# Kernel tuning notes

Measured on AMD Instinct MI355X. Metric: run time of the kernel, lower is better.

## Reference

```python
import jax, jax.numpy as jnp
import numpy as np

INPUT_WINDOW = 2048
HEAD_DIM = 128  # embedding_size // number_of_heads = 2048 // 16
TAU = 1.0
SCALE = 1.0 / ((INPUT_WINDOW * HEAD_DIM) ** 0.5 * TAU)


def setup_inputs() -> dict:
    key = jax.random.key(0)
    # (batch, number_of_series, length_input_window, hidden_dimensionality)
    x = jax.random.normal(key, (8, 16, 2048, 128), dtype=jnp.float32)
    return {"x": x}


def reference(x) -> jnp.ndarray:
    # Q = K = V = x; scores: [B, S, W, W]
    qk = jnp.einsum("bswd,bsud->bswu", x, x) * SCALE
    attn = jax.nn.softmax(qk, axis=-1)
    # dropout(p=0.1) is identity in eval mode
    out = jnp.einsum("bswu,bsud->bswd", attn, x)
    return out
```

## Files before the change

### kernel.cpp

```cpp
#include <hip/hip_runtime.h>
#include <hip/hip_bf16.h>
#include <utility>


#define NSEQ   2048
#define DIM    128
#define KVBLK  32
#define TILES  (NSEQ / KVBLK)
#define IMG    (KVBLK * DIM)
#define EC (1.44269504088896f / 512.0f)

typedef short s8v __attribute__((ext_vector_type(8)));
typedef float f4   __attribute__((ext_vector_type(4)));
typedef float f8v  __attribute__((ext_vector_type(8)));
typedef float f16v __attribute__((ext_vector_type(16)));
typedef unsigned int u2 __attribute__((ext_vector_type(2)));
typedef unsigned int u4 __attribute__((ext_vector_type(4)));

typedef __attribute__((address_space(1))) const void glob_t;
typedef __attribute__((address_space(3))) void lds_t;

__device__ __forceinline__ unsigned pk2(float a, float b) {
    union { __hip_bfloat162 h; unsigned u; } c;
    c.h = __float22bfloat162_rn(make_float2(a, b));
    return c.u;
}
__device__ __forceinline__ int swz32k(int r) { return ((r & 7) ^ ((r >> 3) & 3)) << 3; }
__device__ __forceinline__ int swz(int r) { return ((r & 7) ^ ((r >> 3) & 7)) << 3; }

__global__ __launch_bounds__(256)
void prepass(const float* __restrict__ x, short* __restrict__ wsK,
             short* __restrict__ wsV) {
    const int b = blockIdx.x;
    const float* src = x + (size_t)b * (64 * DIM);
    short* dK = wsK + (size_t)b * 2 * IMG;
    short* dV = wsV + (size_t)b * 2 * IMG;
    const int rw = threadIdx.x >> 4;
    const int cg = threadIdx.x & 15;
    const int tile = rw >> 3;
    const int ul   = 4 * (rw & 7);

    f4 ld[8];
    const float* s = src + (size_t)(4 * rw) * DIM + 8 * cg;
#pragma unroll
    for (int i = 0; i < 4; ++i) {
        ld[2*i]   = *(const f4*)(s + i * DIM);
        ld[2*i+1] = *(const f4*)(s + i * DIM + 4);
    }
#pragma unroll
    for (int i = 0; i < 4; ++i) {
        const int rl = ul + i;
        u4 kv = { pk2(ld[2*i][0],   ld[2*i][1]),   pk2(ld[2*i][2],   ld[2*i][3]),
                  pk2(ld[2*i+1][0], ld[2*i+1][1]), pk2(ld[2*i+1][2], ld[2*i+1][3]) };
        *(u4*)&dK[tile * IMG + ((rl * DIM + 8 * cg) ^ swz32k(rl))] = kv;
    }
#pragma unroll
    for (int j = 0; j < 8; ++j) {
        const int d  = 8 * cg + j;
        const int hi = j >> 2, jj = j & 3;
        u2 vv = { pk2(ld[0 + hi][jj], ld[2 + hi][jj]),
                  pk2(ld[4 + hi][jj], ld[6 + hi][jj]) };
        *(u2*)&dV[tile * IMG + ((d * KVBLK + ul) ^ swz32k(d))] = vv;
    }
}

__global__ __launch_bounds__(256, 3)
void attn_k32p(const float* __restrict__ x, const short* __restrict__ wsK,
               const short* __restrict__ wsV, float* __restrict__ out) {
    const int bid  = blockIdx.x;
    const int wg   = (bid & 7) * 256 + (bid >> 3);
    const int head = wg >> 4;
    const int qb   = wg & 15;

    float* __restrict__ oh = out + (size_t)head * (NSEQ * DIM);
    const short* gK = wsK + (size_t)head * TILES * IMG;
    const short* gV = wsV + (size_t)head * TILES * IMG;

    const int tid  = threadIdx.x;
    const int lane = tid & 63;
    const int wave = tid >> 6;
    const int l31  = lane & 31;
    const int h    = lane >> 5;

    __shared__ __align__(16) short sK [2][IMG];
    __shared__ __align__(16) short sVt[2][IMG];

    const int qw0 = qb * 128 + wave * 32;
    s8v Qf[8];
    {
        const float* qp = x + (size_t)head * (NSEQ * DIM)
                            + (size_t)(qw0 + l31) * DIM + 8 * h;
#pragma unroll
        for (int ks = 0; ks < 8; ++ks) {
            f4 a = *(const f4*)(qp + ks * 16);
            f4 b = *(const f4*)(qp + ks * 16 + 4);
            u4 q = { pk2(a[0] * EC, a[1] * EC), pk2(a[2] * EC, a[3] * EC),
                     pk2(b[0] * EC, b[1] * EC), pk2(b[2] * EC, b[3] * EC) };
            Qf[ks] = *(s8v*)&q;
        }
    }

    f16v accO[4];
#pragma unroll
    for (int dt = 0; dt < 4; ++dt) accO[dt] = (f16v)(0.f);
    float lsum = 0.f;

    const int soff = wave * 1024 + lane * 8;
    auto stage = [&](int b, int t) {
        const short* srcK = gK + (size_t)t * IMG + soff;
        const short* srcV = gV + (size_t)t * IMG + soff;
#pragma unroll
        for (int i = 0; i < 2; ++i) {
            __builtin_amdgcn_global_load_lds((glob_t*)(srcK + i * 512),
                (lds_t*)&sK[b][soff + i * 512], 16, 0, 0);
            __builtin_amdgcn_global_load_lds((glob_t*)(srcV + i * 512),
                (lds_t*)&sVt[b][soff + i * 512], 16, 0, 0);
        }
    };

    stage(0, 0);
    __syncthreads();

    const int kbase = l31 * DIM + 8 * h;
    const int ksz   = swz32k(l31);

    auto body = [&](auto Bc, int T) {
        constexpr int B = decltype(Bc)::value;
        if (T + 1 < TILES) stage(B ^ 1, T + 1);

        f16v aA = (f16v)(0.f), aB = (f16v)(0.f);
        __builtin_amdgcn_s_setprio(1);
#pragma unroll
        for (int ks = 0; ks < 4; ++ks) {
            s8v Kf0 = *(const s8v*)&sK[B][(kbase + (2 * ks)     * 16) ^ ksz];
            s8v Kf1 = *(const s8v*)&sK[B][(kbase + (2 * ks + 1) * 16) ^ ksz];
            aA = __builtin_amdgcn_mfma_f32_32x32x16_bf16(Kf0, Qf[2*ks],   aA, 0, 0, 0);
            aB = __builtin_amdgcn_mfma_f32_32x32x16_bf16(Kf1, Qf[2*ks+1], aB, 0, 0, 0);
        }
        __builtin_amdgcn_s_setprio(0);

        float part0 = 0.f, part1 = 0.f;
        f8v P0, P1;
#pragma unroll
        for (int r = 0; r < 8; ++r) {
            float v = __builtin_amdgcn_exp2f(aA[r] + aB[r]);
            P0[r] = v; part0 += v;
        }
        s8v Pf0;
        {
            unsigned x0 = pk2(P0[0], P0[1]), x1 = pk2(P0[2], P0[3]);
            unsigned y0 = pk2(P0[4], P0[5]), y1 = pk2(P0[6], P0[7]);
            auto t0 = __builtin_amdgcn_permlane32_swap(x0, y0, false, false);
            auto t1 = __builtin_amdgcn_permlane32_swap(x1, y1, false, false);
            u4 w = { (unsigned)t0[0], (unsigned)t1[0], (unsigned)t0[1], (unsigned)t1[1] };
            Pf0 = *(s8v*)&w;
        }

        __builtin_amdgcn_s_setprio(1);
#pragma unroll
        for (int dt = 0; dt < 4; ++dt) {
            const int d = dt * 32 + l31;
            s8v Vf = *(const s8v*)&sVt[B][(d * KVBLK + 8 * h) ^ swz32k(d)];
            accO[dt] = __builtin_amdgcn_mfma_f32_32x32x16_bf16(Pf0, Vf, accO[dt], 0, 0, 0);
        }
        __builtin_amdgcn_s_setprio(0);

#pragma unroll
        for (int r = 0; r < 8; ++r) {
            float v = __builtin_amdgcn_exp2f(aA[8 + r] + aB[8 + r]);
            P1[r] = v; part1 += v;
        }
        s8v Pf1;
        {
            unsigned x0 = pk2(P1[0], P1[1]), x1 = pk2(P1[2], P1[3]);
            unsigned y0 = pk2(P1[4], P1[5]), y1 = pk2(P1[6], P1[7]);
            auto t0 = __builtin_amdgcn_permlane32_swap(x0, y0, false, false);
            auto t1 = __builtin_amdgcn_permlane32_swap(x1, y1, false, false);
            u4 w = { (unsigned)t0[0], (unsigned)t1[0], (unsigned)t0[1], (unsigned)t1[1] };
            Pf1 = *(s8v*)&w;
        }
        lsum += part0 + part1;

        __builtin_amdgcn_s_setprio(1);
#pragma unroll
        for (int dt = 0; dt < 4; ++dt) {
            const int d = dt * 32 + l31;
            s8v Vf = *(const s8v*)&sVt[B][(d * KVBLK + 8 * h + 16) ^ swz32k(d)];
            accO[dt] = __builtin_amdgcn_mfma_f32_32x32x16_bf16(Pf1, Vf, accO[dt], 0, 0, 0);
        }
        __builtin_amdgcn_s_setprio(0);

        __syncthreads();
    };

    for (int tt = 0; tt < TILES; tt += 2) {
        body(std::integral_constant<int, 0>{}, tt);
        body(std::integral_constant<int, 1>{}, tt + 1);
    }

    const float tot = lsum + __shfl_xor(lsum, 32);
    const float inv = 1.f / tot;
#pragma unroll
    for (int r = 0; r < 16; ++r) {
        const int q      = (r & 3) + 8 * (r >> 2) + 4 * h;
        const float invq = __shfl(inv, q, 32);
        float* op = oh + (size_t)(qw0 + q) * DIM + l31;
#pragma unroll
        for (int dt = 0; dt < 4; ++dt)
            op[dt * 32] = accO[dt][r] * invq;
    }
}

__global__ __launch_bounds__(256, 2)
void attn_fwd_fb(const float* __restrict__ x, float* __restrict__ out) {
    const int bid  = blockIdx.x;
    const int wg   = (bid & 7) * 256 + (bid >> 3);
    const int head = wg >> 4;
    const int qb   = wg & 15;
    const float* __restrict__ xh = x   + (size_t)head * (NSEQ * DIM);
    float* __restrict__       oh = out + (size_t)head * (NSEQ * DIM);
    const int tid  = threadIdx.x;
    const int lane = tid & 63;
    const int wave = tid >> 6;
    const int l31  = lane & 31;
    const int h    = lane >> 5;
    __shared__ __align__(16) short sK [64 * DIM];
    __shared__ __align__(16) short sVt[DIM * 64];
    const int qw0 = qb * 128 + wave * 32;
    s8v Qf[8];
    {
        const float* qp = xh + (size_t)(qw0 + l31) * DIM + 8 * h;
#pragma unroll
        for (int ks = 0; ks < 8; ++ks) {
            f4 a = *(const f4*)(qp + ks * 16);
            f4 b = *(const f4*)(qp + ks * 16 + 4);
            u4 q = { pk2(a[0] * EC, a[1] * EC), pk2(a[2] * EC, a[3] * EC),
                     pk2(b[0] * EC, b[1] * EC), pk2(b[2] * EC, b[3] * EC) };
            Qf[ks] = *(s8v*)&q;
        }
    }
    f16v accO[4];
#pragma unroll
    for (int dt = 0; dt < 4; ++dt) accO[dt] = (f16v)(0.f);
    float lsum = 0.f;
    const int rw = tid >> 4;
    const int cg = tid & 15;
    f4 ld[8];
    {
        const float* s = xh + (size_t)(4 * rw) * DIM + 8 * cg;
#pragma unroll
        for (int i = 0; i < 4; ++i) {
            ld[2*i]   = *(const f4*)(s + i * DIM);
            ld[2*i+1] = *(const f4*)(s + i * DIM + 4);
        }
    }
    for (int kv0 = 0; kv0 < NSEQ; kv0 += 64) {
#pragma unroll
        for (int i = 0; i < 4; ++i) {
            const int r = 4 * rw + i;
            u4 kv = { pk2(ld[2*i][0],   ld[2*i][1]),   pk2(ld[2*i][2],   ld[2*i][3]),
                      pk2(ld[2*i+1][0], ld[2*i+1][1]), pk2(ld[2*i+1][2], ld[2*i+1][3]) };
            *(u4*)&sK[(r * DIM + 8 * cg) ^ swz(r)] = kv;
        }
#pragma unroll
        for (int j = 0; j < 8; ++j) {
            const int d  = 8 * cg + j;
            const int hi = j >> 2, jj = j & 3;
            u2 vv = { pk2(ld[0 + hi][jj], ld[2 + hi][jj]),
                      pk2(ld[4 + hi][jj], ld[6 + hi][jj]) };
            *(u2*)&sVt[(d * 64 + 4 * rw) ^ swz(d)] = vv;
        }
        __syncthreads();
        f16v accS[2];
        accS[0] = (f16v)(0.f); accS[1] = (f16v)(0.f);
        __builtin_amdgcn_s_setprio(1);
#pragma unroll
        for (int ut = 0; ut < 2; ++ut) {
            const int r    = ut * 32 + l31;
            const int base = r * DIM + 8 * h;
            const int sz   = swz(r);
#pragma unroll
            for (int ks = 0; ks < 8; ++ks) {
                s8v Kf = *(const s8v*)&sK[(base + ks * 16) ^ sz];
                accS[ut] = __builtin_amdgcn_mfma_f32_32x32x16_bf16(
                    Kf, Qf[ks], accS[ut], 0, 0, 0);
            }
        }
        __builtin_amdgcn_s_setprio(0);
        if (kv0 + 64 < NSEQ) {
            const float* s = xh + (size_t)(kv0 + 64 + 4 * rw) * DIM + 8 * cg;
#pragma unroll
            for (int i = 0; i < 4; ++i) {
                ld[2*i]   = *(const f4*)(s + i * DIM);
                ld[2*i+1] = *(const f4*)(s + i * DIM + 4);
            }
        }
        float part = 0.f;
#pragma unroll
        for (int ut = 0; ut < 2; ++ut)
#pragma unroll
            for (int r = 0; r < 16; ++r) {
                float v = __builtin_amdgcn_exp2f(accS[ut][r]);
                accS[ut][r] = v;
                part += v;
            }
        lsum += part;
        s8v Pf[4];
#pragma unroll
        for (int ks = 0; ks < 4; ++ks) {
#define PP(f) accS[(f) >> 4][(f) & 15]
            unsigned pa0 = pk2(PP(8*ks + 0), PP(8*ks + 1));
            unsigned pa1 = pk2(PP(8*ks + 2), PP(8*ks + 3));
            unsigned pb0 = pk2(PP(8*ks + 4), PP(8*ks + 5));
            unsigned pb1 = pk2(PP(8*ks + 6), PP(8*ks + 7));
#undef PP
            auto t0 = __builtin_amdgcn_permlane32_swap(pa0, pb0, false, false);
            auto t1 = __builtin_amdgcn_permlane32_swap(pa1, pb1, false, false);
            u4 w = { (unsigned)t0[0], (unsigned)t1[0], (unsigned)t0[1], (unsigned)t1[1] };
            Pf[ks] = *(s8v*)&w;
        }
        __builtin_amdgcn_s_setprio(1);
#pragma unroll
        for (int dt = 0; dt < 4; ++dt) {
            const int d    = dt * 32 + l31;
            const int base = d * 64 + 8 * h;
            const int sz   = swz(d);
#pragma unroll
            for (int ks = 0; ks < 4; ++ks) {
                s8v Vf = *(const s8v*)&sVt[(base + ks * 16) ^ sz];
                accO[dt] = __builtin_amdgcn_mfma_f32_32x32x16_bf16(
                    Pf[ks], Vf, accO[dt], 0, 0, 0);
            }
        }
        __builtin_amdgcn_s_setprio(0);
        __syncthreads();
    }
    const float tot = lsum + __shfl_xor(lsum, 32);
    const float inv = 1.f / tot;
#pragma unroll
    for (int r = 0; r < 16; ++r) {
        const int q      = (r & 3) + 8 * (r >> 2) + 4 * h;
        const float invq = __shfl(inv, q, 32);
        float* op = oh + (size_t)(qw0 + q) * DIM + l31;
#pragma unroll
        for (int dt = 0; dt < 4; ++dt)
            op[dt * 32] = accO[dt][r] * invq;
    }
}

extern "C" void kernel_launch(void* const* d_in, const int* in_sizes, int n_in,
                              void* d_out, int out_size, void* d_ws, size_t ws_size,
                              hipStream_t stream) {
    const float* x = (const float*)d_in[0];
    float* out     = (float*)d_out;
    const size_t perImg = (size_t)128 * TILES * IMG;
    const size_t need   = 2 * perImg * sizeof(short);
    if (ws_size >= need) {
        short* wsK = (short*)d_ws;
        short* wsV = wsK + perImg;
        hipLaunchKernelGGL(prepass, dim3(4096), dim3(256), 0, stream, x, wsK, wsV);
        hipLaunchKernelGGL(attn_k32p, dim3(2048), dim3(256), 0, stream, x, wsK, wsV, out);
    } else {
        hipLaunchKernelGGL(attn_fwd_fb, dim3(2048), dim3(256), 0, stream, x, out);
    }
}
```

Baseline: 363.7 us.

## Software-pipeline QK^T of next tile with softmax and PV of current tile

Restructures the attention loop so the QK^T MFMAs for tile T+1 are interleaved with the exp2 and PV MFMAs of tile T, with a prologue and epilogue to match. K and V staging are split so K is prefetched two tiles ahead and V one tile ahead. The goal is to hide exp/VALU latency behind matrix-core work and lengthen the load prefetch distance. In exchange it keeps two score accumulators live, which raises register pressure at an occupancy of 3 waves per SIMD, and it drops the split aA/aB accumulators in favour of one dependent MFMA chain.

Result: faster. 354.3 us (-2.6%).

```diff
diff --git a/kernel.cpp b/kernel.cpp
--- a/kernel.cpp
+++ b/kernel.cpp
@@ -12,7 +12,6 @@
 
 typedef short s8v __attribute__((ext_vector_type(8)));
 typedef float f4   __attribute__((ext_vector_type(4)));
-typedef float f8v  __attribute__((ext_vector_type(8)));
 typedef float f16v __attribute__((ext_vector_type(16)));
 typedef unsigned int u2 __attribute__((ext_vector_type(2)));
 typedef unsigned int u4 __attribute__((ext_vector_type(4)));
@@ -26,7 +25,7 @@
     return c.u;
 }
 __device__ __forceinline__ int swz32k(int r) { return ((r & 7) ^ ((r >> 3) & 3)) << 3; }
-__device__ __forceinline__ int swz(int r) { return ((r & 7) ^ ((r >> 3) & 7)) << 3; }
+__device__ __forceinline__ int swz(int r)    { return ((r & 7) ^ ((r >> 3) & 7)) << 3; }
 
 __global__ __launch_bounds__(256)
 void prepass(const float* __restrict__ x, short* __restrict__ wsK,
@@ -65,7 +64,7 @@
 }
 
 __global__ __launch_bounds__(256, 3)
-void attn_k32p(const float* __restrict__ x, const short* __restrict__ wsK,
+void attn_pipe(const float* __restrict__ x, const short* __restrict__ wsK,
                const short* __restrict__ wsV, float* __restrict__ out) {
     const int bid  = blockIdx.x;
     const int wg   = (bid & 7) * 256 + (bid >> 3);
@@ -106,96 +105,130 @@
     float lsum = 0.f;
 
     const int soff = wave * 1024 + lane * 8;
-    auto stage = [&](int b, int t) {
-        const short* srcK = gK + (size_t)t * IMG + soff;
-        const short* srcV = gV + (size_t)t * IMG + soff;
-#pragma unroll
-        for (int i = 0; i < 2; ++i) {
-            __builtin_amdgcn_global_load_lds((glob_t*)(srcK + i * 512),
+    auto stageK = [&](int b, int t) {
+        const short* src = gK + (size_t)t * IMG + soff;
+#pragma unroll
+        for (int i = 0; i < 2; ++i)
+            __builtin_amdgcn_global_load_lds((glob_t*)(src + i * 512),
                 (lds_t*)&sK[b][soff + i * 512], 16, 0, 0);
-            __builtin_amdgcn_global_load_lds((glob_t*)(srcV + i * 512),
+    };
+    auto stageV = [&](int b, int t) {
+        const short* src = gV + (size_t)t * IMG + soff;
+#pragma unroll
+        for (int i = 0; i < 2; ++i)
+            __builtin_amdgcn_global_load_lds((glob_t*)(src + i * 512),
                 (lds_t*)&sVt[b][soff + i * 512], 16, 0, 0);
-        }
     };
-
-    stage(0, 0);
-    __syncthreads();
 
     const int kbase = l31 * DIM + 8 * h;
     const int ksz   = swz32k(l31);
 
-    auto body = [&](auto Bc, int T) {
-        constexpr int B = decltype(Bc)::value;
-        if (T + 1 < TILES) stage(B ^ 1, T + 1);
-
-        f16v aA = (f16v)(0.f), aB = (f16v)(0.f);
+    stageK(0, 0); stageV(0, 0); stageK(1, 1);
+    __syncthreads();
+
+    f16v accS0 = (f16v)(0.f), accS1;
+    __builtin_amdgcn_s_setprio(1);
+#pragma unroll
+    for (int ks = 0; ks < 8; ++ks) {
+        s8v Kf = *(const s8v*)&sK[0][(kbase + ks * 16) ^ ksz];
+        accS0 = __builtin_amdgcn_mfma_f32_32x32x16_bf16(Kf, Qf[ks], accS0, 0, 0, 0);
+    }
+    __builtin_amdgcn_s_setprio(0);
+    __syncthreads();
+
+    auto body = [&](auto Pc, int T, f16v& aR, f16v& aW) {
+        constexpr int P = decltype(Pc)::value;
+        if (T + 2 < TILES) stageK(P, T + 2);
+        stageV(P ^ 1, T + 1);
+
+        aW = (f16v)(0.f);
+        f16v p;
+        float part = 0.f;
         __builtin_amdgcn_s_setprio(1);
 #pragma unroll
-        for (int ks = 0; ks < 4; ++ks) {
-            s8v Kf0 = *(const s8v*)&sK[B][(kbase + (2 * ks)     * 16) ^ ksz];
-            s8v Kf1 = *(const s8v*)&sK[B][(kbase + (2 * ks + 1) * 16) ^ ksz];
-            aA = __builtin_amdgcn_mfma_f32_32x32x16_bf16(Kf0, Qf[2*ks],   aA, 0, 0, 0);
-            aB = __builtin_amdgcn_mfma_f32_32x32x16_bf16(Kf1, Qf[2*ks+1], aB, 0, 0, 0);
-        }
-        __builtin_amdgcn_s_setprio(0);
-
-        float part0 = 0.f, part1 = 0.f;
-        f8v P0, P1;
-#pragma unroll
-        for (int r = 0; r < 8; ++r) {
-            float v = __builtin_amdgcn_exp2f(aA[r] + aB[r]);
-            P0[r] = v; part0 += v;
-        }
-        s8v Pf0;
+        for (int ks = 0; ks < 8; ++ks) {
+            s8v Kf = *(const s8v*)&sK[P ^ 1][(kbase + ks * 16) ^ ksz];
+            aW = __builtin_amdgcn_mfma_f32_32x32x16_bf16(Kf, Qf[ks], aW, 0, 0, 0);
+            float e0 = __builtin_amdgcn_exp2f(aR[2 * ks]);
+            float e1 = __builtin_amdgcn_exp2f(aR[2 * ks + 1]);
+            p[2 * ks] = e0; p[2 * ks + 1] = e1;
+            part += e0 + e1;
+        }
+        lsum += part;
+
+        s8v Pf0, Pf1;
         {
-            unsigned x0 = pk2(P0[0], P0[1]), x1 = pk2(P0[2], P0[3]);
-            unsigned y0 = pk2(P0[4], P0[5]), y1 = pk2(P0[6], P0[7]);
+            unsigned x0 = pk2(p[0], p[1]), x1 = pk2(p[2], p[3]);
+            unsigned y0 = pk2(p[4], p[5]), y1 = pk2(p[6], p[7]);
             auto t0 = __builtin_amdgcn_permlane32_swap(x0, y0, false, false);
             auto t1 = __builtin_amdgcn_permlane32_swap(x1, y1, false, false);
             u4 w = { (unsigned)t0[0], (unsigned)t1[0], (unsigned)t0[1], (unsigned)t1[1] };
             Pf0 = *(s8v*)&w;
         }
-
-        __builtin_amdgcn_s_setprio(1);
+        {
+            unsigned x0 = pk2(p[8], p[9]),  x1 = pk2(p[10], p[11]);
+            unsigned y0 = pk2(p[12], p[13]), y1 = pk2(p[14], p[15]);
+            auto t0 = __builtin_amdgcn_permlane32_swap(x0, y0, false, false);
+            auto t1 = __builtin_amdgcn_permlane32_swap(x1, y1, false, false);
+            u4 w = { (unsigned)t0[0], (unsigned)t1[0], (unsigned)t0[1], (unsigned)t1[1] };
+            Pf1 = *(s8v*)&w;
+        }
+
 #pragma unroll
         for (int dt = 0; dt < 4; ++dt) {
             const int d = dt * 32 + l31;
-            s8v Vf = *(const s8v*)&sVt[B][(d * KVBLK + 8 * h) ^ swz32k(d)];
-            accO[dt] = __builtin_amdgcn_mfma_f32_32x32x16_bf16(Pf0, Vf, accO[dt], 0, 0, 0);
+            s8v Vf0 = *(const s8v*)&sVt[P][(d * KVBLK + 8 * h)      ^ swz32k(d)];
+            s8v Vf1 = *(const s8v*)&sVt[P][(d * KVBLK + 8 * h + 16) ^ swz32k(d)];
+            accO[dt] = __builtin_amdgcn_mfma_f32_32x32x16_bf16(Pf0, Vf0, accO[dt], 0, 0, 0);
+            accO[dt] = __builtin_amdgcn_mfma_f32_32x32x16_bf16(Pf1, Vf1, accO[dt], 0, 0, 0);
         }
         __builtin_amdgcn_s_setprio(0);
 
-#pragma unroll
-        for (int r = 0; r < 8; ++r) {
-            float v = __builtin_amdgcn_exp2f(aA[8 + r] + aB[8 + r]);
-            P1[r] = v; part1 += v;
-        }
-        s8v Pf1;
+        __syncthreads();
+    };
+
+    for (int tt = 0; tt < 62; tt += 2) {
+        body(std::integral_constant<int, 0>{}, tt,     accS0, accS1);
+        body(std::integral_constant<int, 1>{}, tt + 1, accS1, accS0);
+    }
+    body(std::integral_constant<int, 0>{}, 62, accS0, accS1);
+
+    {
+        f16v p;
+        float part = 0.f;
+#pragma unroll
+        for (int r = 0; r < 16; ++r) {
+            float v = __builtin_amdgcn_exp2f(accS1[r]);
+            p[r] = v; part += v;
+        }
+        lsum += part;
+        s8v Pf0, Pf1;
         {
-            unsigned x0 = pk2(P1[0], P1[1]), x1 = pk2(P1[2], P1[3]);
-            unsigned y0 = pk2(P1[4], P1[5]), y1 = pk2(P1[6], P1[7]);
+            unsigned x0 = pk2(p[0], p[1]), x1 = pk2(p[2], p[3]);
+            unsigned y0 = pk2(p[4], p[5]), y1 = pk2(p[6], p[7]);
             auto t0 = __builtin_amdgcn_permlane32_swap(x0, y0, false, false);
             auto t1 = __builtin_amdgcn_permlane32_swap(x1, y1, false, false);
             u4 w = { (unsigned)t0[0], (unsigned)t1[0], (unsigned)t0[1], (unsigned)t1[1] };
+            Pf0 = *(s8v*)&w;
+        }
+        {
+            unsigned x0 = pk2(p[8], p[9]),  x1 = pk2(p[10], p[11]);
+            unsigned y0 = pk2(p[12], p[13]), y1 = pk2(p[14], p[15]);
+            auto t0 = __builtin_amdgcn_permlane32_swap(x0, y0, false, false);
+            auto t1 = __builtin_amdgcn_permlane32_swap(x1, y1, false, false);
+            u4 w = { (unsigned)t0[0], (unsigned)t1[0], (unsigned)t0[1], (unsigned)t1[1] };
             Pf1 = *(s8v*)&w;
         }
-        lsum += part0 + part1;
-
         __builtin_amdgcn_s_setprio(1);
 #pragma unroll
         for (int dt = 0; dt < 4; ++dt) {
             const int d = dt * 32 + l31;
-            s8v Vf = *(const s8v*)&sVt[B][(d * KVBLK + 8 * h + 16) ^ swz32k(d)];
-            accO[dt] = __builtin_amdgcn_mfma_f32_32x32x16_bf16(Pf1, Vf, accO[dt], 0, 0, 0);
+            s8v Vf0 = *(const s8v*)&sVt[1][(d * KVBLK + 8 * h)      ^ swz32k(d)];
+            s8v Vf1 = *(const s8v*)&sVt[1][(d * KVBLK + 8 * h + 16) ^ swz32k(d)];
+            accO[dt] = __builtin_amdgcn_mfma_f32_32x32x16_bf16(Pf0, Vf0, accO[dt], 0, 0, 0);
+            accO[dt] = __builtin_amdgcn_mfma_f32_32x32x16_bf16(Pf1, Vf1, accO[dt], 0, 0, 0);
         }
         __builtin_amdgcn_s_setprio(0);
-
-        __syncthreads();
-    };
-
-    for (int tt = 0; tt < TILES; tt += 2) {
-        body(std::integral_constant<int, 0>{}, tt);
-        body(std::integral_constant<int, 1>{}, tt + 1);
     }
 
     const float tot = lsum + __shfl_xor(lsum, 32);
@@ -359,7 +392,7 @@
         short* wsK = (short*)d_ws;
         short* wsV = wsK + perImg;
         hipLaunchKernelGGL(prepass, dim3(4096), dim3(256), 0, stream, x, wsK, wsV);
-        hipLaunchKernelGGL(attn_k32p, dim3(2048), dim3(256), 0, stream, x, wsK, wsV, out);
+        hipLaunchKernelGGL(attn_pipe, dim3(2048), dim3(256), 0, stream, x, wsK, wsV, out);
     } else {
         hipLaunchKernelGGL(attn_fwd_fb, dim3(2048), dim3(256), 0, stream, x, out);
     }
```

## Triple-buffer K/V tiles with counted vmcnt waits and a single QK accumulator

Applied to the files above, without the earlier changes.

Replaces the double-buffered K/V staging with a three-slot ring that keeps two tiles in flight. Each iteration waits with s_waitcnt vmcnt(4) plus a raw s_barrier, instead of a full __syncthreads that drains all loads. The QK product now uses one accumulator chain of 8 MFMAs rather than two interleaved chains. The P·V MFMAs are grouped after the full softmax instead of being interleaved with the exp work. This hides global-to-LDS latency better, but the LDS footprint grows by half, which may hurt 3-blocks/CU occupancy, and the single dependent MFMA chain lengthens QK latency.

Measured after the change: 355.7 us. 1.02x faster.

```diff
diff --git a/kernel.cpp b/kernel.cpp
--- a/kernel.cpp
+++ b/kernel.cpp
@@ -1,6 +1,5 @@
 #include <hip/hip_runtime.h>
 #include <hip/hip_bf16.h>
-#include <utility>
 
 
 #define NSEQ   2048
@@ -12,7 +11,6 @@
 
 typedef short s8v __attribute__((ext_vector_type(8)));
 typedef float f4   __attribute__((ext_vector_type(4)));
-typedef float f8v  __attribute__((ext_vector_type(8)));
 typedef float f16v __attribute__((ext_vector_type(16)));
 typedef unsigned int u2 __attribute__((ext_vector_type(2)));
 typedef unsigned int u4 __attribute__((ext_vector_type(4)));
@@ -26,7 +24,7 @@
     return c.u;
 }
 __device__ __forceinline__ int swz32k(int r) { return ((r & 7) ^ ((r >> 3) & 3)) << 3; }
-__device__ __forceinline__ int swz(int r) { return ((r & 7) ^ ((r >> 3) & 7)) << 3; }
+__device__ __forceinline__ int swz(int r)    { return ((r & 7) ^ ((r >> 3) & 7)) << 3; }
 
 __global__ __launch_bounds__(256)
 void prepass(const float* __restrict__ x, short* __restrict__ wsK,
@@ -65,8 +63,8 @@
 }
 
 __global__ __launch_bounds__(256, 3)
-void attn_k32p(const float* __restrict__ x, const short* __restrict__ wsK,
-               const short* __restrict__ wsV, float* __restrict__ out) {
+void attn_cnt(const float* __restrict__ x, const short* __restrict__ wsK,
+              const short* __restrict__ wsV, float* __restrict__ out) {
     const int bid  = blockIdx.x;
     const int wg   = (bid & 7) * 256 + (bid >> 3);
     const int head = wg >> 4;
@@ -82,8 +80,8 @@
     const int l31  = lane & 31;
     const int h    = lane >> 5;
 
-    __shared__ __align__(16) short sK [2][IMG];
-    __shared__ __align__(16) short sVt[2][IMG];
+    __shared__ __align__(16) short sK [3][IMG];
+    __shared__ __align__(16) short sVt[3][IMG];
 
     const int qw0 = qb * 128 + wave * 32;
     s8v Qf[8];
@@ -110,93 +108,92 @@
         const short* srcK = gK + (size_t)t * IMG + soff;
         const short* srcV = gV + (size_t)t * IMG + soff;
 #pragma unroll
-        for (int i = 0; i < 2; ++i) {
+        for (int i = 0; i < 2; ++i)
             __builtin_amdgcn_global_load_lds((glob_t*)(srcK + i * 512),
                 (lds_t*)&sK[b][soff + i * 512], 16, 0, 0);
+#pragma unroll
+        for (int i = 0; i < 2; ++i)
             __builtin_amdgcn_global_load_lds((glob_t*)(srcV + i * 512),
                 (lds_t*)&sVt[b][soff + i * 512], 16, 0, 0);
-        }
     };
-
-    stage(0, 0);
-    __syncthreads();
 
     const int kbase = l31 * DIM + 8 * h;
     const int ksz   = swz32k(l31);
 
-    auto body = [&](auto Bc, int T) {
-        constexpr int B = decltype(Bc)::value;
-        if (T + 1 < TILES) stage(B ^ 1, T + 1);
-
-        f16v aA = (f16v)(0.f), aB = (f16v)(0.f);
+    auto compute = [&](int b) {
+        const short* bK = &sK[b][0];
+        const short* bV = &sVt[b][0];
+        f16v accS = (f16v)(0.f);
         __builtin_amdgcn_s_setprio(1);
 #pragma unroll
-        for (int ks = 0; ks < 4; ++ks) {
-            s8v Kf0 = *(const s8v*)&sK[B][(kbase + (2 * ks)     * 16) ^ ksz];
-            s8v Kf1 = *(const s8v*)&sK[B][(kbase + (2 * ks + 1) * 16) ^ ksz];
-            aA = __builtin_amdgcn_mfma_f32_32x32x16_bf16(Kf0, Qf[2*ks],   aA, 0, 0, 0);
-            aB = __builtin_amdgcn_mfma_f32_32x32x16_bf16(Kf1, Qf[2*ks+1], aB, 0, 0, 0);
+        for (int ks = 0; ks < 8; ++ks) {
+            s8v Kf = *(const s8v*)&bK[(kbase + ks * 16) ^ ksz];
+            accS = __builtin_amdgcn_mfma_f32_32x32x16_bf16(Kf, Qf[ks], accS, 0, 0, 0);
         }
         __builtin_amdgcn_s_setprio(0);
 
-        float part0 = 0.f, part1 = 0.f;
-        f8v P0, P1;
-#pragma unroll
-        for (int r = 0; r < 8; ++r) {
-            float v = __builtin_amdgcn_exp2f(aA[r] + aB[r]);
-            P0[r] = v; part0 += v;
-        }
-        s8v Pf0;
+        f16v p;
+        float part = 0.f;
+#pragma unroll
+        for (int r = 0; r < 16; ++r) {
+            float v = __builtin_amdgcn_exp2f(accS[r]);
+            p[r] = v; part += v;
+        }
+        lsum += part;
+
+        s8v Pf0, Pf1;
         {
-            unsigned x0 = pk2(P0[0], P0[1]), x1 = pk2(P0[2], P0[3]);
-            unsigned y0 = pk2(P0[4], P0[5]), y1 = pk2(P0[6], P0[7]);
+            unsigned x0 = pk2(p[0], p[1]), x1 = pk2(p[2], p[3]);
+            unsigned y0 = pk2(p[4], p[5]), y1 = pk2(p[6], p[7]);
             auto t0 = __builtin_amdgcn_permlane32_swap(x0, y0, false, false);
             auto t1 = __builtin_amdgcn_permlane32_swap(x1, y1, false, false);
             u4 w = { (unsigned)t0[0], (unsigned)t1[0], (unsigned)t0[1], (unsigned)t1[1] };
             Pf0 = *(s8v*)&w;
         }
-
-        __builtin_amdgcn_s_setprio(1);
-#pragma unroll
-        for (int dt = 0; dt < 4; ++dt) {
-            const int d = dt * 32 + l31;
-            s8v Vf = *(const s8v*)&sVt[B][(d * KVBLK + 8 * h) ^ swz32k(d)];
-            accO[dt] = __builtin_amdgcn_mfma_f32_32x32x16_bf16(Pf0, Vf, accO[dt], 0, 0, 0);
-        }
-        __builtin_amdgcn_s_setprio(0);
-
-#pragma unroll
-        for (int r = 0; r < 8; ++r) {
-            float v = __builtin_amdgcn_exp2f(aA[8 + r] + aB[8 + r]);
-            P1[r] = v; part1 += v;
-        }
-        s8v Pf1;
         {
-            unsigned x0 = pk2(P1[0], P1[1]), x1 = pk2(P1[2], P1[3]);
-            unsigned y0 = pk2(P1[4], P1[5]), y1 = pk2(P1[6], P1[7]);
+            unsigned x0 = pk2(p[8], p[9]),  x1 = pk2(p[10], p[11]);
+            unsigned y0 = pk2(p[12], p[13]), y1 = pk2(p[14], p[15]);
             auto t0 = __builtin_amdgcn_permlane32_swap(x0, y0, false, false);
             auto t1 = __builtin_amdgcn_permlane32_swap(x1, y1, false, false);
             u4 w = { (unsigned)t0[0], (unsigned)t1[0], (unsigned)t0[1], (unsigned)t1[1] };
             Pf1 = *(s8v*)&w;
         }
-        lsum += part0 + part1;
 
         __builtin_amdgcn_s_setprio(1);
 #pragma unroll
         for (int dt = 0; dt < 4; ++dt) {
             const int d = dt * 32 + l31;
-            s8v Vf = *(const s8v*)&sVt[B][(d * KVBLK + 8 * h + 16) ^ swz32k(d)];
-            accO[dt] = __builtin_amdgcn_mfma_f32_32x32x16_bf16(Pf1, Vf, accO[dt], 0, 0, 0);
+            s8v Vf0 = *(const s8v*)&bV[(d * KVBLK + 8 * h)      ^ swz32k(d)];
+            s8v Vf1 = *(const s8v*)&bV[(d * KVBLK + 8 * h + 16) ^ swz32k(d)];
+            accO[dt] = __builtin_amdgcn_mfma_f32_32x32x16_bf16(Pf0, Vf0, accO[dt], 0, 0, 0);
+            accO[dt] = __builtin_amdgcn_mfma_f32_32x32x16_bf16(Pf1, Vf1, accO[dt], 0, 0, 0);
         }
         __builtin_amdgcn_s_setprio(0);
-
-        __syncthreads();
     };
 
-    for (int tt = 0; tt < TILES; tt += 2) {
-        body(std::integral_constant<int, 0>{}, tt);
-        body(std::integral_constant<int, 1>{}, tt + 1);
-    }
+    stage(0, 0); stage(1, 1);
+    asm volatile("s_waitcnt vmcnt(4)" ::: "memory");
+    __builtin_amdgcn_s_barrier();
+    __builtin_amdgcn_sched_barrier(0);
+
+    int cur = 0, stg = 2;
+    for (int T = 0; T < TILES - 2; ++T) {
+        stage(stg, T + 2);
+        compute(cur);
+        asm volatile("s_waitcnt vmcnt(4)" ::: "memory");
+        __builtin_amdgcn_s_barrier();
+        __builtin_amdgcn_sched_barrier(0);
+        cur = (cur == 2) ? 0 : cur + 1;
+        stg = (stg == 2) ? 0 : stg + 1;
+    }
+
+    compute(cur);
+    asm volatile("s_waitcnt vmcnt(0)" ::: "memory");
+    __builtin_amdgcn_s_barrier();
+    __builtin_amdgcn_sched_barrier(0);
+    cur = (cur == 2) ? 0 : cur + 1;
+
+    compute(cur);
 
     const float tot = lsum + __shfl_xor(lsum, 32);
     const float inv = 1.f / tot;
@@ -359,7 +356,7 @@
         short* wsK = (short*)d_ws;
         short* wsV = wsK + perImg;
         hipLaunchKernelGGL(prepass, dim3(4096), dim3(256), 0, stream, x, wsK, wsV);
-        hipLaunchKernelGGL(attn_k32p, dim3(2048), dim3(256), 0, stream, x, wsK, wsV, out);
+        hipLaunchKernelGGL(attn_cnt, dim3(2048), dim3(256), 0, stream, x, wsK, wsV, out);
     } else {
         hipLaunchKernelGGL(attn_fwd_fb, dim3(2048), dim3(256), 0, stream, x, out);
     }
```
